# Optimization experiments

Measured on AMD Instinct MI355X. Metric: run time of the kernel, lower is better.

Reference implementation:

```python
import jax, jax.numpy as jnp
import numpy as np

N, E, F_IN, H0, H1 = 50000, 800000, 128, 128, 64


def setup_inputs() -> dict:
    key = jax.random.key(0)
    k1, k2, k3, k4, k5, k6 = jax.random.split(key, 6)
    node_features = jax.random.normal(k1, (N, F_IN), dtype=jnp.float32)
    edges = jax.random.randint(k2, (E, 2), 0, N, dtype=jnp.int64)
    # GCNConv params (glorot-ish scale)
    W1 = jax.random.normal(k3, (F_IN, H0), dtype=jnp.float32) / np.sqrt(F_IN)
    b1 = jnp.zeros((H0,), dtype=jnp.float32)
    W2 = jax.random.normal(k4, (H0, H1), dtype=jnp.float32) / np.sqrt(H0)
    b2 = jnp.zeros((H1,), dtype=jnp.float32)
    return {"node_features": node_features, "edges": edges,
            "W1": W1, "b1": b1, "W2": W2, "b2": b2}


def reference(node_features, edges, W1, b1, W2, b2):
    # GCNConv: out = D^{-1/2} (A + I) D^{-1/2} (X W) + b, with self-loops.
    n = node_features.shape[0]
    ei = edges.T  # [2, E] like edge_index.t() in the torch code
    self_idx = jnp.arange(n, dtype=ei.dtype)
    src = jnp.concatenate([ei[0], self_idx])  # [E+N]
    dst = jnp.concatenate([ei[1], self_idx])  # [E+N]
    deg = jnp.zeros((n,), node_features.dtype).at[dst].add(1.0)  # >=1 (self-loops)
    dinv = jax.lax.rsqrt(deg)
    norm = (dinv[src] * dinv[dst])[:, None]  # [E+N, 1]

    def gcn(x, W, b):
        h = x @ W                      # dense transform [n, d_out]
        msg = h[src] * norm            # gather + scale  [E+N, d_out]
        agg = jax.ops.segment_sum(msg, dst, num_segments=n)  # scatter-add
        return agg + b

    x = jax.nn.relu(gcn(node_features, W1, b1))
    # F.dropout(training=self.training): identity in eval mode (deterministic ref)
    x = gcn(x, W2, b2)
    return x
```

## Files before the change

### kernel.cpp

```cpp
#include <hip/hip_runtime.h>
#include <hip/hip_bf16.h>


#define NCHUNK 128

#define OFF_ROWSTART (size_t)0x0
#define OFF_DINV     (size_t)0x40000
#define OFF_BLOCKSUM (size_t)0x80000
#define OFF_FLAG     (size_t)0x80800
#define OFF_LRANK    (size_t)0x81000
#define OFF_CSR      (size_t)0x150000
#define OFF_H        (size_t)0x300000
#define OFF_W1T      (size_t)0xA00000
#define OFF_W2T      (size_t)0xA10000
#define OFF_BUFA     (size_t)0xB00000
#define OFF_BUFB     (size_t)0x1800000

typedef short bf16x8 __attribute__((ext_vector_type(8)));
typedef float f32x4 __attribute__((ext_vector_type(4)));

__device__ __forceinline__ float2 bf2f(unsigned u) {
    float2 r;
    r.x = __uint_as_float(u << 16);
    r.y = __uint_as_float(u & 0xffff0000u);
    return r;
}
__device__ __forceinline__ unsigned f2bf(float a, float b) {
    __hip_bfloat162 h = __float22bfloat162_rn(make_float2(a, b));
    union { __hip_bfloat162 h; unsigned u; } cv;
    cv.h = h;
    return cv.u;
}

__global__ __launch_bounds__(256) void k_hist(const int* __restrict__ e32, int E,
                                              int chunk, int n,
                                              unsigned char* __restrict__ lrank,
                                              unsigned char* __restrict__ H,
                                              int* __restrict__ flag,
                                              const float* __restrict__ W1,
                                              const float* __restrict__ W2,
                                              unsigned short* __restrict__ W1T,
                                              unsigned short* __restrict__ W2T) {
    const int t = threadIdx.x, b = blockIdx.x;
    if (b >= NCHUNK) {
        const int bb = b - NCHUNK;
        const int k0 = (t & 15) * 8;
        if (bb < 8) {
            int nn = bb * 16 + (t >> 4);
            float w[8];
#pragma unroll
            for (int j = 0; j < 8; ++j) w[j] = W1[(size_t)(k0 + j) * 128 + nn];
            uint4 q;
            q.x = f2bf(w[0], w[1]); q.y = f2bf(w[2], w[3]);
            q.z = f2bf(w[4], w[5]); q.w = f2bf(w[6], w[7]);
            *reinterpret_cast<uint4*>(&W1T[(size_t)nn * 128 + k0]) = q;
        } else {
            int nn = (bb - 8) * 16 + (t >> 4);
            float w[8];
#pragma unroll
            for (int j = 0; j < 8; ++j) w[j] = W2[(size_t)(k0 + j) * 64 + nn];
            uint4 q;
            q.x = f2bf(w[0], w[1]); q.y = f2bf(w[2], w[3]);
            q.z = f2bf(w[4], w[5]); q.w = f2bf(w[6], w[7]);
            *reinterpret_cast<uint4*>(&W2T[(size_t)nn * 128 + k0]) = q;
        }
        return;
    }
    __shared__ unsigned h[12544];
    __shared__ int anyv;
    const int nw = (n + 3) >> 2;
    if (t == 0) anyv = 0;
    for (int i = t; i < nw; i += 256) h[i] = 0u;
    __syncthreads();
    const int e0 = b * chunk, e1 = min(E, e0 + chunk);
    int v = 0;
    const int lim = min(e1, e0 + 2048);
    for (int e = e0 + t; e < lim; e += 256) v |= e32[2 * e + 1];
    if (v) atomicOr(&anyv, 1);
    __syncthreads();
    const int f = (anyv == 0) ? 1 : 0;
    if (b == 0 && t == 0) *flag = f;
    for (int e = e0 + t; e < e1; e += 256) {
        int dst;
        if (f) dst = reinterpret_cast<const int4*>(e32)[e].z;
        else   dst = reinterpret_cast<const int2*>(e32)[e].y;
        int sh = (dst & 3) << 3;
        unsigned old = atomicAdd(&h[dst >> 2], 1u << sh);
        lrank[e] = (unsigned char)((old >> sh) & 0xffu);
    }
    __syncthreads();
    unsigned* Hp = reinterpret_cast<unsigned*>(H);
    const size_t wbase = (size_t)b * (size_t)(n >> 2);
    for (int i = t; i < (n >> 2); i += 256) Hp[wbase + i] = h[i];
}

__global__ __launch_bounds__(256) void k_mergescan(
        unsigned char* __restrict__ H, int n,
        float* __restrict__ dinv, int* __restrict__ rowstart,
        int* __restrict__ blocksum) {
    __shared__ int sh[256];
    const int t = threadIdx.x;
    const int bin0 = blockIdx.x * 1024 + 4 * t;
    int s0 = 0, s1 = 0, s2 = 0, s3 = 0;
    if (bin0 < n) {
        unsigned* Hp = reinterpret_cast<unsigned*>(H);
        const size_t wstride = (size_t)(n >> 2);
        const size_t widx = (size_t)(bin0 >> 2);
#pragma unroll 8
        for (int b = 0; b < NCHUNK; ++b) {
            size_t idx = (size_t)b * wstride + widx;
            unsigned w = Hp[idx];
            Hp[idx] = (unsigned)s0 | ((unsigned)s1 << 8) |
                      ((unsigned)s2 << 16) | ((unsigned)s3 << 24);
            s0 += (int)(w & 0xffu);
            s1 += (int)((w >> 8) & 0xffu);
            s2 += (int)((w >> 16) & 0xffu);
            s3 += (int)((w >> 24) & 0xffu);
        }
        float4 dv;
        dv.x = rsqrtf((float)s0 + 1.0f);
        dv.y = rsqrtf((float)s1 + 1.0f);
        dv.z = rsqrtf((float)s2 + 1.0f);
        dv.w = rsqrtf((float)s3 + 1.0f);
        *reinterpret_cast<float4*>(dinv + bin0) = dv;
    }
    int tot = s0 + s1 + s2 + s3;
    sh[t] = tot;
    __syncthreads();
    for (int off = 1; off < 256; off <<= 1) {
        int add = (t >= off) ? sh[t - off] : 0;
        __syncthreads();
        sh[t] += add;
        __syncthreads();
    }
    if (bin0 < n) {
        int ex = sh[t] - tot;
        int4 rs;
        rs.x = ex;
        rs.y = ex + s0;
        rs.z = ex + s0 + s1;
        rs.w = ex + s0 + s1 + s2;
        *reinterpret_cast<int4*>(rowstart + bin0) = rs;
    }
    if (t == 255) blocksum[blockIdx.x] = sh[255];
}

__global__ void k_scan3(int* __restrict__ rowstart, int n,
                        const int* __restrict__ blocksum, int nb, int E) {
    __shared__ int bs[65];
    int t = threadIdx.x;
    if (t < nb) bs[t + 1] = blocksum[t];
    if (t == 0) bs[0] = 0;
    __syncthreads();
    if (t == 0) {
        int s = 0;
        for (int k = 1; k <= nb; ++k) { s += bs[k]; bs[k] = s; }
    }
    __syncthreads();
    int i = blockIdx.x * 256 + t;
    if (i < n) rowstart[i] += bs[i >> 10];
    if (i == 0) rowstart[n] = E;
}

__global__ void k_fill(const int* __restrict__ e32, int E, int chunk,
                       const int* __restrict__ flag,
                       const int* __restrict__ rowstart,
                       const unsigned char* __restrict__ H, int n,
                       const unsigned char* __restrict__ lrank,
                       unsigned short* __restrict__ csr) {
    int e = blockIdx.x * 256 + threadIdx.x;
    if (e >= E) return;
    int b = blockIdx.x / (chunk >> 8);
    int f = *flag;
    int src, dst;
    if (f) { int4 v = reinterpret_cast<const int4*>(e32)[e]; src = v.x; dst = v.z; }
    else   { int2 v = reinterpret_cast<const int2*>(e32)[e]; src = v.x; dst = v.y; }
    csr[rowstart[dst] + (int)H[(size_t)b * n + dst] + (int)lrank[e]] =
        (unsigned short)src;
}

__global__ __launch_bounds__(256) void k_gemm1m(const float* __restrict__ X,
                                                const unsigned short* __restrict__ W1T,
                                                const float* __restrict__ dinv,
                                                unsigned short* __restrict__ out,
                                                int n) {
    __shared__ unsigned short Xs[64 * 136];
    __shared__ unsigned short Ws[128 * 136];
    const int t = threadIdx.x;
    const int row0 = blockIdx.x * 64;
#pragma unroll
    for (int it = 0; it < 8; ++it) {
        int i = t + it * 256;
        int r = i >> 4, c8 = i & 15;
        *reinterpret_cast<uint4*>(&Ws[r * 136 + c8 * 8]) =
            *reinterpret_cast<const uint4*>(&W1T[(size_t)r * 128 + c8 * 8]);
    }
#pragma unroll
    for (int it = 0; it < 8; ++it) {
        int i = t + it * 256;
        int r = i >> 5, c4 = i & 31;
        int gr = row0 + r;
        float4 v = make_float4(0.f, 0.f, 0.f, 0.f);
        if (gr < n) v = *reinterpret_cast<const float4*>(&X[(size_t)gr * 128 + c4 * 4]);
        uint2 q;
        q.x = f2bf(v.x, v.y);
        q.y = f2bf(v.z, v.w);
        *reinterpret_cast<uint2*>(&Xs[r * 136 + c4 * 4]) = q;
    }
    __syncthreads();
    const int w = t >> 6, lane = t & 63;
    const int m = lane & 15, kg = lane >> 4;
    f32x4 acc[8] = {};
#pragma unroll
    for (int kt = 0; kt < 128; kt += 32) {
        bf16x8 a = *reinterpret_cast<const bf16x8*>(&Xs[(w * 16 + m) * 136 + kt + kg * 8]);
#pragma unroll
        for (int j = 0; j < 8; ++j) {
            bf16x8 bb = *reinterpret_cast<const bf16x8*>(&Ws[(j * 16 + m) * 136 + kt + kg * 8]);
            acc[j] = __builtin_amdgcn_mfma_f32_16x16x32_bf16(a, bb, acc[j], 0, 0, 0);
        }
    }
    const int rbase = row0 + w * 16 + kg * 4;
#pragma unroll
    for (int r = 0; r < 4; ++r) {
        int gr = rbase + r;
        if (gr < n) {
            float dv = dinv[gr];
#pragma unroll
            for (int j = 0; j < 8; ++j)
                out[(size_t)gr * 128 + j * 16 + m] =
                    (unsigned short)(f2bf(acc[j][r] * dv, 0.f) & 0xffffu);
        }
    }
}

__global__ __launch_bounds__(256) void k_gemm2m(const unsigned short* __restrict__ X1,
                                                const unsigned short* __restrict__ W2T,
                                                const float* __restrict__ dinv,
                                                unsigned short* __restrict__ out,
                                                int n) {
    __shared__ unsigned short Xs[64 * 136];
    __shared__ unsigned short Ws[64 * 136];
    const int t = threadIdx.x;
    const int row0 = blockIdx.x * 64;
#pragma unroll
    for (int it = 0; it < 4; ++it) {
        int i = t + it * 256;
        int r = i >> 4, c8 = i & 15;
        *reinterpret_cast<uint4*>(&Ws[r * 136 + c8 * 8]) =
            *reinterpret_cast<const uint4*>(&W2T[(size_t)r * 128 + c8 * 8]);
    }
#pragma unroll
    for (int it = 0; it < 4; ++it) {
        int i = t + it * 256;
        int r = i >> 4, c8 = i & 15;
        int gr = row0 + r;
        uint4 q = make_uint4(0u, 0u, 0u, 0u);
        if (gr < n) q = *reinterpret_cast<const uint4*>(&X1[(size_t)gr * 128 + c8 * 8]);
        *reinterpret_cast<uint4*>(&Xs[r * 136 + c8 * 8]) = q;
    }
    __syncthreads();
    const int w = t >> 6, lane = t & 63;
    const int m = lane & 15, kg = lane >> 4;
    f32x4 acc[4] = {};
#pragma unroll
    for (int kt = 0; kt < 128; kt += 32) {
        bf16x8 a = *reinterpret_cast<const bf16x8*>(&Xs[(w * 16 + m) * 136 + kt + kg * 8]);
#pragma unroll
        for (int j = 0; j < 4; ++j) {
            bf16x8 bb = *reinterpret_cast<const bf16x8*>(&Ws[(j * 16 + m) * 136 + kt + kg * 8]);
            acc[j] = __builtin_amdgcn_mfma_f32_16x16x32_bf16(a, bb, acc[j], 0, 0, 0);
        }
    }
    const int rbase = row0 + w * 16 + kg * 4;
#pragma unroll
    for (int r = 0; r < 4; ++r) {
        int gr = rbase + r;
        if (gr < n) {
            float dv = dinv[gr];
#pragma unroll
            for (int j = 0; j < 4; ++j)
                out[(size_t)gr * 64 + j * 16 + m] =
                    (unsigned short)(f2bf(acc[j][r] * dv, 0.f) & 0xffffu);
        }
    }
}

__global__ __launch_bounds__(256) void k_spmm128(
        const unsigned* __restrict__ H32, const int* __restrict__ rowstart,
        const unsigned short* __restrict__ csr, const float* __restrict__ dinv,
        const float* __restrict__ bias, unsigned* __restrict__ out, int n) {
    int node = blockIdx.x * 8 + (threadIdx.x >> 5);
    if (node >= n) return;
    int f2 = threadIdx.x & 31;
    const uint2* H2 = reinterpret_cast<const uint2*>(H32);
    float di = dinv[node];
    uint2 sv = H2[(size_t)node * 32 + f2];
    float2 a0 = bf2f(sv.x), a1 = bf2f(sv.y);
    float acc0 = a0.x, acc1 = a0.y, acc2 = a1.x, acc3 = a1.y;
    int s0 = rowstart[node], s1 = rowstart[node + 1];
    for (int j = s0; j < s1; j += 8) {
        int srcs[8];
        uint2 uu[8];
#pragma unroll
        for (int u = 0; u < 8; ++u) srcs[u] = csr[min(j + u, s1 - 1)];
#pragma unroll
        for (int u = 0; u < 8; ++u) uu[u] = H2[(size_t)srcs[u] * 32 + f2];
#pragma unroll
        for (int u = 0; u < 8; ++u) {
            float2 f0 = bf2f(uu[u].x), f1 = bf2f(uu[u].y);
            bool ok = (j + u) < s1;
            acc0 += ok ? f0.x : 0.f;
            acc1 += ok ? f0.y : 0.f;
            acc2 += ok ? f1.x : 0.f;
            acc3 += ok ? f1.y : 0.f;
        }
    }
    float4 b = reinterpret_cast<const float4*>(bias)[f2];
    float o0 = fmaxf(fmaf(di, acc0, b.x), 0.f);
    float o1 = fmaxf(fmaf(di, acc1, b.y), 0.f);
    float o2 = fmaxf(fmaf(di, acc2, b.z), 0.f);
    float o3 = fmaxf(fmaf(di, acc3, b.w), 0.f);
    uint2 q;
    q.x = f2bf(o0, o1);
    q.y = f2bf(o2, o3);
    reinterpret_cast<uint2*>(out)[(size_t)node * 32 + f2] = q;
}

__global__ __launch_bounds__(256) void k_spmm64(
        const unsigned* __restrict__ H32, const int* __restrict__ rowstart,
        const unsigned short* __restrict__ csr, const float* __restrict__ dinv,
        const float* __restrict__ bias, float* __restrict__ out, int n) {
    int node = blockIdx.x * 16 + (threadIdx.x >> 4);
    if (node >= n) return;
    int f2 = threadIdx.x & 15;
    const uint2* H2 = reinterpret_cast<const uint2*>(H32);
    float di = dinv[node];
    uint2 sv = H2[(size_t)node * 16 + f2];
    float2 a0 = bf2f(sv.x), a1 = bf2f(sv.y);
    float acc0 = a0.x, acc1 = a0.y, acc2 = a1.x, acc3 = a1.y;
    int s0 = rowstart[node], s1 = rowstart[node + 1];
    for (int j = s0; j < s1; j += 8) {
        int srcs[8];
        uint2 uu[8];
#pragma unroll
        for (int u = 0; u < 8; ++u) srcs[u] = csr[min(j + u, s1 - 1)];
#pragma unroll
        for (int u = 0; u < 8; ++u) uu[u] = H2[(size_t)srcs[u] * 16 + f2];
#pragma unroll
        for (int u = 0; u < 8; ++u) {
            float2 f0 = bf2f(uu[u].x), f1 = bf2f(uu[u].y);
            bool ok = (j + u) < s1;
            acc0 += ok ? f0.x : 0.f;
            acc1 += ok ? f0.y : 0.f;
            acc2 += ok ? f1.x : 0.f;
            acc3 += ok ? f1.y : 0.f;
        }
    }
    float4 b = reinterpret_cast<const float4*>(bias)[f2];
    float4 o;
    o.x = fmaf(di, acc0, b.x);
    o.y = fmaf(di, acc1, b.y);
    o.z = fmaf(di, acc2, b.z);
    o.w = fmaf(di, acc3, b.w);
    reinterpret_cast<float4*>(out)[(size_t)node * 16 + f2] = o;
}

extern "C" void kernel_launch(void* const* d_in, const int* in_sizes, int n_in,
                              void* d_out, int out_size, void* d_ws, size_t ws_size,
                              hipStream_t stream) {
    const float* X   = (const float*)d_in[0];
    const int*   e32 = (const int*)d_in[1];
    const float* W1  = (const float*)d_in[2];
    const float* b1  = (const float*)d_in[3];
    const float* W2  = (const float*)d_in[4];
    const float* b2  = (const float*)d_in[5];
    float* out = (float*)d_out;

    const int n = in_sizes[0] / 128;
    const int E = in_sizes[1] / 2;
    const int chunk = (((E + NCHUNK - 1) / NCHUNK) + 255) & ~255;

    char* ws = (char*)d_ws;
    int*            rowstart = (int*)(ws + OFF_ROWSTART);
    float*          dinv     = (float*)(ws + OFF_DINV);
    int*            blocksum = (int*)(ws + OFF_BLOCKSUM);
    int*            flag     = (int*)(ws + OFF_FLAG);
    unsigned char*  lrank    = (unsigned char*)(ws + OFF_LRANK);
    unsigned short* csr      = (unsigned short*)(ws + OFF_CSR);
    unsigned char*  H        = (unsigned char*)(ws + OFF_H);
    unsigned short* W1T      = (unsigned short*)(ws + OFF_W1T);
    unsigned short* W2T      = (unsigned short*)(ws + OFF_W2T);
    unsigned short* bufA     = (unsigned short*)(ws + OFF_BUFA);
    unsigned*       bufB     = (unsigned*)(ws + OFF_BUFB);

    const int NB   = (n + 255) / 256;
    const int NBms = (n + 1023) / 1024;
    const int EB   = (E + 255) / 256;
    const int RB   = (n + 63) / 64;

    k_hist<<<NCHUNK + 12, 256, 0, stream>>>(e32, E, chunk, n, lrank, H, flag,
                                            W1, W2, W1T, W2T);
    k_mergescan<<<NBms, 256, 0, stream>>>(H, n, dinv, rowstart, blocksum);
    k_scan3<<<NB, 256, 0, stream>>>(rowstart, n, blocksum, NBms, E);
    k_fill<<<EB, 256, 0, stream>>>(e32, E, chunk, flag, rowstart, H, n, lrank, csr);

    k_gemm1m<<<RB, 256, 0, stream>>>(X, W1T, dinv, bufA, n);
    k_spmm128<<<(n + 7) / 8, 256, 0, stream>>>((const unsigned*)bufA, rowstart, csr,
                                               dinv, b1, bufB, n);
    k_gemm2m<<<RB, 256, 0, stream>>>((const unsigned short*)bufB, W2T, dinv, bufA, n);
    k_spmm64<<<(n + 15) / 16, 256, 0, stream>>>((const unsigned*)bufA, rowstart, csr,
                                                dinv, b2, out, n);
}
```

Baseline: 127.8 us.

## Stage per-chunk histogram in LDS for CSR fill and split layer-1 SpMM by feature halves

The CSR fill kernel now runs one pair of blocks per edge chunk. Each block copies that chunk's per-node histogram row (n bytes) into shared memory, so offsets come from LDS instead of scattered global byte loads. The layer-1 SpMM is split into two launches, each covering 64 of the 128 features, so each pass gathers a smaller working set of H and should hit cache more often. The costs are a full n-byte LDS copy in every fill block, a 50 KB LDS footprint that limits occupancy, and reading the CSR indices twice in the split SpMM. The fixed-size shared buffer and the n>>4 copy loop also assume n fits in 50176 bytes and is a multiple of 16.

```diff
diff --git a/kernel.cpp b/kernel.cpp
--- a/kernel.cpp
+++ b/kernel.cpp
@@ -162,21 +162,34 @@
     if (i == 0) rowstart[n] = E;
 }
 
-__global__ void k_fill(const int* __restrict__ e32, int E, int chunk,
-                       const int* __restrict__ flag,
-                       const int* __restrict__ rowstart,
-                       const unsigned char* __restrict__ H, int n,
-                       const unsigned char* __restrict__ lrank,
-                       unsigned short* __restrict__ csr) {
-    int e = blockIdx.x * 256 + threadIdx.x;
-    if (e >= E) return;
-    int b = blockIdx.x / (chunk >> 8);
-    int f = *flag;
-    int src, dst;
-    if (f) { int4 v = reinterpret_cast<const int4*>(e32)[e]; src = v.x; dst = v.z; }
-    else   { int2 v = reinterpret_cast<const int2*>(e32)[e]; src = v.x; dst = v.y; }
-    csr[rowstart[dst] + (int)H[(size_t)b * n + dst] + (int)lrank[e]] =
-        (unsigned short)src;
+__global__ __launch_bounds__(256) void k_fill(const int* __restrict__ e32, int E,
+                                              int chunk,
+                                              const int* __restrict__ flag,
+                                              const int* __restrict__ rowstart,
+                                              const unsigned char* __restrict__ H,
+                                              int n,
+                                              const unsigned char* __restrict__ lrank,
+                                              unsigned short* __restrict__ csr) {
+    __shared__ unsigned char hs[50176];
+    const int t = threadIdx.x;
+    const int b = blockIdx.x >> 1;
+    const int half = blockIdx.x & 1;
+    {
+        const uint4* src = reinterpret_cast<const uint4*>(H + (size_t)b * n);
+        uint4* dst = reinterpret_cast<uint4*>(hs);
+        for (int i = t; i < (n >> 4); i += 256) dst[i] = src[i];
+    }
+    __syncthreads();
+    const int f = *flag;
+    const int hchunk = chunk >> 1;
+    const int e0 = b * chunk + half * hchunk;
+    const int e1 = min(E, e0 + hchunk);
+    for (int e = e0 + t; e < e1; e += 256) {
+        int src, dst;
+        if (f) { int4 v = reinterpret_cast<const int4*>(e32)[e]; src = v.x; dst = v.z; }
+        else   { int2 v = reinterpret_cast<const int2*>(e32)[e]; src = v.x; dst = v.y; }
+        csr[rowstart[dst] + (int)hs[dst] + (int)lrank[e]] = (unsigned short)src;
+    }
 }
 
 __global__ __launch_bounds__(256) void k_gemm1m(const float* __restrict__ X,
@@ -286,16 +299,17 @@
     }
 }
 
-__global__ __launch_bounds__(256) void k_spmm128(
+__global__ __launch_bounds__(256) void k_spmm128h(
         const unsigned* __restrict__ H32, const int* __restrict__ rowstart,
         const unsigned short* __restrict__ csr, const float* __restrict__ dinv,
-        const float* __restrict__ bias, unsigned* __restrict__ out, int n) {
-    int node = blockIdx.x * 8 + (threadIdx.x >> 5);
+        const float* __restrict__ bias, unsigned* __restrict__ out, int n,
+        int foff) {
+    int node = blockIdx.x * 16 + (threadIdx.x >> 4);
     if (node >= n) return;
-    int f2 = threadIdx.x & 31;
+    int fq = (foff >> 2) + (threadIdx.x & 15);
     const uint2* H2 = reinterpret_cast<const uint2*>(H32);
     float di = dinv[node];
-    uint2 sv = H2[(size_t)node * 32 + f2];
+    uint2 sv = H2[(size_t)node * 32 + fq];
     float2 a0 = bf2f(sv.x), a1 = bf2f(sv.y);
     float acc0 = a0.x, acc1 = a0.y, acc2 = a1.x, acc3 = a1.y;
     int s0 = rowstart[node], s1 = rowstart[node + 1];
@@ -305,7 +319,7 @@
 #pragma unroll
         for (int u = 0; u < 8; ++u) srcs[u] = csr[min(j + u, s1 - 1)];
 #pragma unroll
-        for (int u = 0; u < 8; ++u) uu[u] = H2[(size_t)srcs[u] * 32 + f2];
+        for (int u = 0; u < 8; ++u) uu[u] = H2[(size_t)srcs[u] * 32 + fq];
 #pragma unroll
         for (int u = 0; u < 8; ++u) {
             float2 f0 = bf2f(uu[u].x), f1 = bf2f(uu[u].y);
@@ -316,7 +330,7 @@
             acc3 += ok ? f1.y : 0.f;
         }
     }
-    float4 b = reinterpret_cast<const float4*>(bias)[f2];
+    float4 b = reinterpret_cast<const float4*>(bias)[fq];
     float o0 = fmaxf(fmaf(di, acc0, b.x), 0.f);
     float o1 = fmaxf(fmaf(di, acc1, b.y), 0.f);
     float o2 = fmaxf(fmaf(di, acc2, b.z), 0.f);
@@ -324,7 +338,7 @@
     uint2 q;
     q.x = f2bf(o0, o1);
     q.y = f2bf(o2, o3);
-    reinterpret_cast<uint2*>(out)[(size_t)node * 32 + f2] = q;
+    reinterpret_cast<uint2*>(out)[(size_t)node * 32 + fq] = q;
 }
 
 __global__ __launch_bounds__(256) void k_spmm64(
@@ -379,7 +393,7 @@
 
     const int n = in_sizes[0] / 128;
     const int E = in_sizes[1] / 2;
-    const int chunk = (((E + NCHUNK - 1) / NCHUNK) + 255) & ~255;
+    const int chunk = (((E + NCHUNK - 1) / NCHUNK) + 511) & ~511;
 
     char* ws = (char*)d_ws;
     int*            rowstart = (int*)(ws + OFF_ROWSTART);
@@ -396,18 +410,20 @@
 
     const int NB   = (n + 255) / 256;
     const int NBms = (n + 1023) / 1024;
-    const int EB   = (E + 255) / 256;
     const int RB   = (n + 63) / 64;
 
     k_hist<<<NCHUNK + 12, 256, 0, stream>>>(e32, E, chunk, n, lrank, H, flag,
                                             W1, W2, W1T, W2T);
     k_mergescan<<<NBms, 256, 0, stream>>>(H, n, dinv, rowstart, blocksum);
     k_scan3<<<NB, 256, 0, stream>>>(rowstart, n, blocksum, NBms, E);
-    k_fill<<<EB, 256, 0, stream>>>(e32, E, chunk, flag, rowstart, H, n, lrank, csr);
+    k_fill<<<NCHUNK * 2, 256, 0, stream>>>(e32, E, chunk, flag, rowstart, H, n,
+                                           lrank, csr);
 
     k_gemm1m<<<RB, 256, 0, stream>>>(X, W1T, dinv, bufA, n);
-    k_spmm128<<<(n + 7) / 8, 256, 0, stream>>>((const unsigned*)bufA, rowstart, csr,
-                                               dinv, b1, bufB, n);
+    k_spmm128h<<<(n + 15) / 16, 256, 0, stream>>>((const unsigned*)bufA, rowstart,
+                                                  csr, dinv, b1, bufB, n, 0);
+    k_spmm128h<<<(n + 15) / 16, 256, 0, stream>>>((const unsigned*)bufA, rowstart,
+                                                  csr, dinv, b1, bufB, n, 64);
     k_gemm2m<<<RB, 256, 0, stream>>>((const unsigned short*)bufB, W2T, dinv, bufA, n);
     k_spmm64<<<(n + 15) / 16, 256, 0, stream>>>((const unsigned*)bufA, rowstart, csr,
                                                 dinv, b2, out, n);
```

Result: no change. 129.5 us (+1.3%).
